# Kernel tuning notes

Hardware: AMD Instinct MI355X
Metric: run time of the kernel (lower is better)

## Reference

```python
import jax, jax.numpy as jnp
import numpy as np

NEG_BIG = -9.0e15  # mask value from original code (-9000000000000000.0)


def setup_inputs() -> dict:
    key = jax.random.key(0)
    k1, k2, k3, k4, k5 = jax.random.split(key, 5)
    B, N, M, D = 32, 1024, 1024, 128
    input1 = jax.random.normal(k1, (B, N, D), dtype=jnp.float32)
    input2 = jax.random.normal(k2, (B, M, D), dtype=jnp.float32)
    adj = jax.random.randint(k3, (B, N, M), 0, 2, dtype=jnp.int32)
    # xavier_normal on (D,1): std = gain*sqrt(2/(fan_in+fan_out)) = 1.414*sqrt(2/(D+1))
    std = 1.414 * np.sqrt(2.0 / (D + 1))
    a1 = jax.random.normal(k4, (D, 1), dtype=jnp.float32) * std
    a2 = jax.random.normal(k5, (D, 1), dtype=jnp.float32) * std
    return {"input1": input1, "input2": input2, "adj": adj, "a1": a1, "a2": a2}


def reference(input1, input2, adj, a1, a2):
    h, g = input1, input2
    # e1: (B,N,1), e2: (B,1,M); broadcast add replaces the repeat() calls
    e1 = jnp.matmul(h, a1)                      # (B,N,1)
    e2 = jnp.matmul(g, a2).transpose(0, 2, 1)   # (B,1,M)
    e = jax.nn.leaky_relu(e1 + e2, negative_slope=0.2)  # (B,N,M)
    attention = jnp.where(adj > 0, e, NEG_BIG)
    attention = jax.nn.softmax(attention, axis=2)
    attention = jnp.where(jnp.isnan(attention), 0.0, attention)
    # per-batch loop in original builds adj_[b,i,j] = adj[b,i,:].sum(); vectorized:
    deg = jnp.sum(adj, axis=2, keepdims=True).astype(attention.dtype)  # (B,N,1)
    attention = attention * deg
    h_prime = jnp.matmul(attention, g)          # (B,N,D)
    return h_prime
```

## Files before the change

### kernel.cpp

```cpp
#include <hip/hip_runtime.h>

#define BB 32
#define NN 1024
#define MM 1024
#define DD 128

typedef __attribute__((ext_vector_type(4))) float f32x4;
typedef __attribute__((ext_vector_type(8))) __bf16 bf16x8;
typedef unsigned short ushort_t;
typedef unsigned int uint_t;

#define L2E 1.44269504f

__device__ __forceinline__ unsigned f2bf(float x) {
    unsigned u = __builtin_bit_cast(unsigned, x);
    return (u + 0x7fffu + ((u >> 16) & 1u)) >> 16;
}

#define GLOAD16(gp, lp)                                                     \
    __builtin_amdgcn_global_load_lds(                                       \
        (const __attribute__((address_space(1))) unsigned int*)(gp),        \
        (__attribute__((address_space(3))) unsigned int*)(lp), 16, 0, 0)

__global__ __launch_bounds__(256) void prep(
    const float* __restrict__ g, const float* __restrict__ h,
    const float* __restrict__ a1, const float* __restrict__ a2,
    ushort_t* __restrict__ gq, float* __restrict__ e1,
    float* __restrict__ e2B, float* __restrict__ e2D)
{
    __shared__ ushort_t tl[DD][66];
    int b = blockIdx.y, m0 = blockIdx.x * 64, t = threadIdx.x;

    #pragma unroll
    for (int i = 0; i < 8; i++) {
        int idx = i * 256 + t;
        int m = idx >> 5;
        int c4 = (idx & 31) * 4;
        float4 v = *(const float4*)(h + ((size_t)(b * NN + m0 + m)) * DD + c4);
        float4 av = *(const float4*)(a1 + c4);
        float p = v.x * av.x + v.y * av.y + v.z * av.z + v.w * av.w;
        #pragma unroll
        for (int s = 16; s; s >>= 1) p += __shfl_xor(p, s);
        if ((t & 31) == 0) e1[b * NN + m0 + m] = p;
    }
    #pragma unroll
    for (int i = 0; i < 8; i++) {
        int idx = i * 256 + t;
        int m = idx >> 5;
        int c4 = (idx & 31) * 4;
        float4 v = *(const float4*)(g + ((size_t)(b * MM + m0 + m)) * DD + c4);
        tl[c4 + 0][m] = (ushort_t)f2bf(v.x);
        tl[c4 + 1][m] = (ushort_t)f2bf(v.y);
        tl[c4 + 2][m] = (ushort_t)f2bf(v.z);
        tl[c4 + 3][m] = (ushort_t)f2bf(v.w);
        float4 av = *(const float4*)(a2 + c4);
        float p = v.x * av.x + v.y * av.y + v.z * av.z + v.w * av.w;
        #pragma unroll
        for (int s = 16; s; s >>= 1) p += __shfl_xor(p, s);
        if ((t & 31) == 0) {
            e2B[b * MM + m0 + m] = __builtin_amdgcn_exp2f(L2E * p);
            e2D[b * MM + m0 + m] = __builtin_amdgcn_exp2f(0.2f * L2E * p);
        }
    }
    __syncthreads();
    #pragma unroll
    for (int i = 0; i < 4; i++) {
        int idx = i * 256 + t;
        int d = idx >> 3;
        int c = (idx & 7) * 8;
        int4 o;
        o.x = (int)((unsigned)tl[d][c + 0] | ((unsigned)tl[d][c + 1] << 16));
        o.y = (int)((unsigned)tl[d][c + 2] | ((unsigned)tl[d][c + 3] << 16));
        o.z = (int)((unsigned)tl[d][c + 4] | ((unsigned)tl[d][c + 5] << 16));
        o.w = (int)((unsigned)tl[d][c + 6] | ((unsigned)tl[d][c + 7] << 16));
        int mg = m0 + c;
        *(int4*)(gq + (((size_t)((b * 32 + (mg >> 5)) * DD + d)) << 5) + (mg & 31)) = o;
    }
}

__global__ __launch_bounds__(256, 2) void attn_tiled(
    const int* __restrict__ adj, const ushort_t* __restrict__ gq,
    const float* __restrict__ e1, const float* __restrict__ e2B,
    const float* __restrict__ e2D, float* __restrict__ out)
{
    __shared__ __align__(16) float BfS[MM];
    __shared__ __align__(16) float DfS[MM];
    __shared__ __align__(16) int adjS[4][64 * 32];
    __shared__ __align__(16) ushort_t gqS[4][128 * 32];

    int b = blockIdx.y, n0 = blockIdx.x * 64, t = threadIdx.x;
    int wid = t >> 6, lane = t & 63;
    int rlo = lane & 15, hh = lane >> 4;
    int r = wid * 16 + rlo;
    int r8 = r & 7;

    *(float4*)(&BfS[t * 4]) = *(const float4*)(e2B + b * MM + t * 4);
    *(float4*)(&DfS[t * 4]) = *(const float4*)(e2D + b * MM + t * 4);
    float e1r = e1[b * NN + n0 + r];
    float An   = __builtin_amdgcn_exp2f(L2E * e1r);
    float Cn   = __builtin_amdgcn_exp2f(0.2f * L2E * e1r);
    float invA = __builtin_amdgcn_exp2f(-L2E * e1r);
    __syncthreads();

    const int* adjb = adj + (size_t)(b * NN + n0) * MM;
    const ushort_t* gqb = gq + (size_t)b * (32 * DD * 32);

    int adi0 = t, adi1 = t + 256;
    int arow0 = adi0 >> 3, aseg0 = (adi0 & 7) ^ (arow0 & 7);
    int arow1 = adi1 >> 3, aseg1 = (adi1 & 7) ^ (arow1 & 7);
    int gd0 = adi0 >> 2, gseg0 = (adi0 & 3) ^ ((gd0 >> 1) & 3);
    int gd1 = adi1 >> 2, gseg1 = (adi1 & 3) ^ ((gd1 >> 1) & 3);

#define STAGE(P, K) do {                                                    \
        GLOAD16(adjb + (size_t)arow0 * MM + (K) * 32 + aseg0 * 4,           \
                &adjS[P][adi0 * 4]);                                        \
        GLOAD16(adjb + (size_t)arow1 * MM + (K) * 32 + aseg1 * 4,           \
                &adjS[P][adi1 * 4]);                                        \
        GLOAD16(gqb + (size_t)(K) * 4096 + gd0 * 32 + gseg0 * 8,            \
                &gqS[P][adi0 * 8]);                                         \
        GLOAD16(gqb + (size_t)(K) * 4096 + gd1 * 32 + gseg1 * 8,            \
                &gqS[P][adi1 * 8]);                                         \
    } while (0)

    f32x4 acc[8];
    #pragma unroll
    for (int j = 0; j < 8; j++) acc[j] = (f32x4){0.f, 0.f, 0.f, 0.f};
    float zl = 0.f;
    int dcnt = 0;

#define COMPUTE(P, K) do {                                                  \
        int4 a0 = *(const int4*)(&adjS[P][r * 32 + ((2 * hh) ^ r8) * 4]);   \
        int4 a1 = *(const int4*)(&adjS[P][r * 32 + ((2 * hh + 1) ^ r8) * 4]);\
        float4 b0 = *(const float4*)(&BfS[(K) * 32 + 8 * hh]);              \
        float4 b1 = *(const float4*)(&BfS[(K) * 32 + 8 * hh + 4]);          \
        float4 d0 = *(const float4*)(&DfS[(K) * 32 + 8 * hh]);              \
        float4 d1 = *(const float4*)(&DfS[(K) * 32 + 8 * hh + 4]);          \
        float Bv[8] = {b0.x, b0.y, b0.z, b0.w, b1.x, b1.y, b1.z, b1.w};     \
        float Dv[8] = {d0.x, d0.y, d0.z, d0.w, d1.x, d1.y, d1.z, d1.w};     \
        int   ax[8] = {a0.x, a0.y, a0.z, a0.w, a1.x, a1.y, a1.z, a1.w};     \
        bf16x8 af;                                                          \
        _Pragma("unroll")                                                   \
        for (int jj = 0; jj < 8; jj++) {                                    \
            float val = (Bv[jj] > invA) ? Bv[jj] * An : Dv[jj] * Cn;        \
            float wv = (ax[jj] > 0) ? val : 0.f;                            \
            zl += wv;                                                       \
            dcnt += ax[jj];                                                 \
            af[jj] = (__bf16)wv;                                            \
        }                                                                   \
        _Pragma("unroll")                                                   \
        for (int j = 0; j < 8; j++) {                                       \
            int d = j * 16 + rlo;                                           \
            int4 bv = *(const int4*)(                                       \
                &gqS[P][d * 32 + (hh ^ ((rlo >> 1) & 3)) * 8]);             \
            acc[j] = __builtin_amdgcn_mfma_f32_16x16x32_bf16(               \
                         af, __builtin_bit_cast(bf16x8, bv), acc[j], 0,0,0);\
        }                                                                   \
    } while (0)

    STAGE(0, 0); STAGE(1, 1); STAGE(2, 2);

    for (int k = 0; k < 30; ++k) {
        asm volatile("s_waitcnt vmcnt(8)" ::: "memory");
        __builtin_amdgcn_s_barrier();
        __builtin_amdgcn_sched_barrier(0);
        if (k < 29) STAGE((k + 3) & 3, k + 3);
        COMPUTE(k & 3, k);
    }
    asm volatile("s_waitcnt vmcnt(4)" ::: "memory");
    __builtin_amdgcn_s_barrier();
    __builtin_amdgcn_sched_barrier(0);
    COMPUTE(2, 30);
    asm volatile("s_waitcnt vmcnt(0)" ::: "memory");
    __builtin_amdgcn_s_barrier();
    __builtin_amdgcn_sched_barrier(0);
    COMPUTE(3, 31);

#undef COMPUTE
#undef STAGE

    zl += __shfl_xor(zl, 16); zl += __shfl_xor(zl, 32);
    dcnt += __shfl_xor(dcnt, 16); dcnt += __shfl_xor(dcnt, 32);
    float sc = (dcnt > 0) ? ((float)dcnt / zl) : 0.f;

    float scr[4];
    #pragma unroll
    for (int rg = 0; rg < 4; rg++) scr[rg] = __shfl(sc, 4 * hh + rg);

    float* ob = out + ((size_t)(b * NN + n0 + wid * 16)) * DD + rlo;
    #pragma unroll
    for (int j = 0; j < 8; j++)
        #pragma unroll
        for (int rg = 0; rg < 4; rg++)
            ob[(size_t)(4 * hh + rg) * DD + j * 16] = acc[j][rg] * scr[rg];
}

extern "C" void kernel_launch(void* const* d_in, const int* in_sizes, int n_in,
                              void* d_out, int out_size, void* d_ws, size_t ws_size,
                              hipStream_t stream) {
    const float* h   = (const float*)d_in[0];
    const float* g   = (const float*)d_in[1];
    const int*   adj = (const int*)d_in[2];
    const float* a1  = (const float*)d_in[3];
    const float* a2  = (const float*)d_in[4];
    float* out = (float*)d_out;

    char* ws = (char*)d_ws;
    float*    e1  = (float*)(ws);
    float*    e2B = (float*)(ws + (128u << 10));
    float*    e2D = (float*)(ws + (256u << 10));
    ushort_t* gq  = (ushort_t*)(ws + (512u << 10));

    prep<<<dim3(MM / 64, BB), 256, 0, stream>>>(g, h, a1, a2, gq, e1, e2B, e2D);
    attn_tiled<<<dim3(NN / 64, BB), 256, 0, stream>>>(adj, gq, e1, e2B, e2D, out);
}
```

Measured before the change: 48.15 us.

## Switch to double-buffered 64-wide K tiles with one barrier per two MFMA steps

```diff
diff --git a/kernel.cpp b/kernel.cpp
--- a/kernel.cpp
+++ b/kernel.cpp
@@ -85,14 +85,13 @@
 {
     __shared__ __align__(16) float BfS[MM];
     __shared__ __align__(16) float DfS[MM];
-    __shared__ __align__(16) int adjS[4][64 * 32];
-    __shared__ __align__(16) ushort_t gqS[4][128 * 32];
+    __shared__ __align__(16) int adjS[2][64 * 64];
+    __shared__ __align__(16) ushort_t gqS[2][2 * 128 * 32];
 
     int b = blockIdx.y, n0 = blockIdx.x * 64, t = threadIdx.x;
     int wid = t >> 6, lane = t & 63;
     int rlo = lane & 15, hh = lane >> 4;
     int r = wid * 16 + rlo;
-    int r8 = r & 7;
 
     *(float4*)(&BfS[t * 4]) = *(const float4*)(e2B + b * MM + t * 4);
     *(float4*)(&DfS[t * 4]) = *(const float4*)(e2D + b * MM + t * 4);
@@ -105,21 +104,32 @@
     const int* adjb = adj + (size_t)(b * NN + n0) * MM;
     const ushort_t* gqb = gq + (size_t)b * (32 * DD * 32);
 
-    int adi0 = t, adi1 = t + 256;
-    int arow0 = adi0 >> 3, aseg0 = (adi0 & 7) ^ (arow0 & 7);
-    int arow1 = adi1 >> 3, aseg1 = (adi1 & 7) ^ (arow1 & 7);
-    int gd0 = adi0 >> 2, gseg0 = (adi0 & 3) ^ ((gd0 >> 1) & 3);
-    int gd1 = adi1 >> 2, gseg1 = (adi1 & 3) ^ ((gd1 >> 1) & 3);
+    int adi[4], aoff[4];
+    #pragma unroll
+    for (int i = 0; i < 4; i++) {
+        adi[i] = t + i * 256;
+        int arow = adi[i] >> 4, aseg = (adi[i] & 15) ^ (arow & 15);
+        aoff[i] = arow * MM + aseg * 4;
+    }
+    int gtile[4], goff[4];
+    #pragma unroll
+    for (int i = 0; i < 4; i++) {
+        int di = t + i * 256;
+        gtile[i] = di >> 9;
+        int idx = di & 511;
+        int gd = idx >> 2, gseg = (idx & 3) ^ ((gd >> 1) & 3);
+        goff[i] = gd * 32 + gseg * 8;
+    }
 
 #define STAGE(P, K) do {                                                    \
-        GLOAD16(adjb + (size_t)arow0 * MM + (K) * 32 + aseg0 * 4,           \
-                &adjS[P][adi0 * 4]);                                        \
-        GLOAD16(adjb + (size_t)arow1 * MM + (K) * 32 + aseg1 * 4,           \
-                &adjS[P][adi1 * 4]);                                        \
-        GLOAD16(gqb + (size_t)(K) * 4096 + gd0 * 32 + gseg0 * 8,            \
-                &gqS[P][adi0 * 8]);                                         \
-        GLOAD16(gqb + (size_t)(K) * 4096 + gd1 * 32 + gseg1 * 8,            \
-                &gqS[P][adi1 * 8]);                                         \
+        _Pragma("unroll")                                                   \
+        for (int i = 0; i < 4; i++)                                         \
+            GLOAD16(adjb + (size_t)aoff[i] + (K) * 64,                      \
+                    &adjS[P][adi[i] * 4]);                                  \
+        _Pragma("unroll")                                                   \
+        for (int i = 0; i < 4; i++)                                         \
+            GLOAD16(gqb + (size_t)(2 * (K) + gtile[i]) * 4096 + goff[i],    \
+                    &gqS[P][(t + i * 256) * 8]);                            \
     } while (0)
 
     f32x4 acc[8];
@@ -128,13 +138,16 @@
     float zl = 0.f;
     int dcnt = 0;
 
-#define COMPUTE(P, K) do {                                                  \
-        int4 a0 = *(const int4*)(&adjS[P][r * 32 + ((2 * hh) ^ r8) * 4]);   \
-        int4 a1 = *(const int4*)(&adjS[P][r * 32 + ((2 * hh + 1) ^ r8) * 4]);\
-        float4 b0 = *(const float4*)(&BfS[(K) * 32 + 8 * hh]);              \
-        float4 b1 = *(const float4*)(&BfS[(K) * 32 + 8 * hh + 4]);          \
-        float4 d0 = *(const float4*)(&DfS[(K) * 32 + 8 * hh]);              \
-        float4 d1 = *(const float4*)(&DfS[(K) * 32 + 8 * hh + 4]);          \
+#define KSTEP(P, K, KS) do {                                                \
+        int4 a0 = *(const int4*)(                                           \
+            &adjS[P][r * 64 + (((KS) * 8 + 2 * hh) ^ rlo) * 4]);            \
+        int4 a1 = *(const int4*)(                                           \
+            &adjS[P][r * 64 + (((KS) * 8 + 2 * hh + 1) ^ rlo) * 4]);        \
+        int mo = (K) * 64 + (KS) * 32 + 8 * hh;                             \
+        float4 b0 = *(const float4*)(&BfS[mo]);                             \
+        float4 b1 = *(const float4*)(&BfS[mo + 4]);                         \
+        float4 d0 = *(const float4*)(&DfS[mo]);                             \
+        float4 d1 = *(const float4*)(&DfS[mo + 4]);                         \
         float Bv[8] = {b0.x, b0.y, b0.z, b0.w, b1.x, b1.y, b1.z, b1.w};     \
         float Dv[8] = {d0.x, d0.y, d0.z, d0.w, d1.x, d1.y, d1.z, d1.w};     \
         int   ax[8] = {a0.x, a0.y, a0.z, a0.w, a1.x, a1.y, a1.z, a1.w};     \
@@ -150,32 +163,25 @@
         _Pragma("unroll")                                                   \
         for (int j = 0; j < 8; j++) {                                       \
             int d = j * 16 + rlo;                                           \
-            int4 bv = *(const int4*)(                                       \
-                &gqS[P][d * 32 + (hh ^ ((rlo >> 1) & 3)) * 8]);             \
+            int4 bv = *(const int4*)(&gqS[P][(KS) * 4096 + d * 32 +         \
+                                             (hh ^ ((rlo >> 1) & 3)) * 8]); \
             acc[j] = __builtin_amdgcn_mfma_f32_16x16x32_bf16(               \
                          af, __builtin_bit_cast(bf16x8, bv), acc[j], 0,0,0);\
         }                                                                   \
     } while (0)
 
-    STAGE(0, 0); STAGE(1, 1); STAGE(2, 2);
-
-    for (int k = 0; k < 30; ++k) {
-        asm volatile("s_waitcnt vmcnt(8)" ::: "memory");
+    STAGE(0, 0);
+
+    for (int k = 0; k < 16; ++k) {
+        asm volatile("s_waitcnt vmcnt(0)" ::: "memory");
         __builtin_amdgcn_s_barrier();
         __builtin_amdgcn_sched_barrier(0);
-        if (k < 29) STAGE((k + 3) & 3, k + 3);
-        COMPUTE(k & 3, k);
-    }
-    asm volatile("s_waitcnt vmcnt(4)" ::: "memory");
-    __builtin_amdgcn_s_barrier();
-    __builtin_amdgcn_sched_barrier(0);
-    COMPUTE(2, 30);
-    asm volatile("s_waitcnt vmcnt(0)" ::: "memory");
-    __builtin_amdgcn_s_barrier();
-    __builtin_amdgcn_sched_barrier(0);
-    COMPUTE(3, 31);
-
-#undef COMPUTE
+        if (k < 15) STAGE((k + 1) & 1, k + 1);
+        KSTEP(k & 1, k, 0);
+        KSTEP(k & 1, k, 1);
+    }
+
+#undef KSTEP
 #undef STAGE
 
     zl += __shfl_xor(zl, 16); zl += __shfl_xor(zl, 32);
```

Measured after the change: 50.28 us. +4.4%, slower.

## Split M reduction across two thread halves with 512-thread blocks

Applied to the files above, without the earlier changes.

```diff
diff --git a/kernel.cpp b/kernel.cpp
--- a/kernel.cpp
+++ b/kernel.cpp
@@ -78,48 +78,51 @@
     }
 }
 
-__global__ __launch_bounds__(256, 2) void attn_tiled(
+__global__ __launch_bounds__(512, 4) void attn_tiled(
     const int* __restrict__ adj, const ushort_t* __restrict__ gq,
     const float* __restrict__ e1, const float* __restrict__ e2B,
     const float* __restrict__ e2D, float* __restrict__ out)
 {
     __shared__ __align__(16) float BfS[MM];
     __shared__ __align__(16) float DfS[MM];
-    __shared__ __align__(16) int adjS[4][64 * 32];
-    __shared__ __align__(16) ushort_t gqS[4][128 * 32];
+    __shared__ __align__(16) int adjS[2][2][64 * 32];
+    __shared__ __align__(16) ushort_t gqS[2][2][128 * 32];
 
     int b = blockIdx.y, n0 = blockIdx.x * 64, t = threadIdx.x;
-    int wid = t >> 6, lane = t & 63;
+    int half = t >> 8;
+    int tt = t & 255;
+    int wid4 = tt >> 6, lane = t & 63;
     int rlo = lane & 15, hh = lane >> 4;
-    int r = wid * 16 + rlo;
-    int r8 = r & 7;
-
-    *(float4*)(&BfS[t * 4]) = *(const float4*)(e2B + b * MM + t * 4);
-    *(float4*)(&DfS[t * 4]) = *(const float4*)(e2D + b * MM + t * 4);
+    int r = wid4 * 16 + rlo;
+    int c0 = half * 16;
+
+    if (half == 0)
+        *(float4*)(&BfS[tt * 4]) = *(const float4*)(e2B + b * MM + tt * 4);
+    else
+        *(float4*)(&DfS[tt * 4]) = *(const float4*)(e2D + b * MM + tt * 4);
     float e1r = e1[b * NN + n0 + r];
     float An   = __builtin_amdgcn_exp2f(L2E * e1r);
     float Cn   = __builtin_amdgcn_exp2f(0.2f * L2E * e1r);
     float invA = __builtin_amdgcn_exp2f(-L2E * e1r);
-    __syncthreads();
 
     const int* adjb = adj + (size_t)(b * NN + n0) * MM;
     const ushort_t* gqb = gq + (size_t)b * (32 * DD * 32);
 
-    int adi0 = t, adi1 = t + 256;
+    int adi0 = tt, adi1 = tt + 256;
     int arow0 = adi0 >> 3, aseg0 = (adi0 & 7) ^ (arow0 & 7);
     int arow1 = adi1 >> 3, aseg1 = (adi1 & 7) ^ (arow1 & 7);
     int gd0 = adi0 >> 2, gseg0 = (adi0 & 3) ^ ((gd0 >> 1) & 3);
     int gd1 = adi1 >> 2, gseg1 = (adi1 & 3) ^ ((gd1 >> 1) & 3);
 
-#define STAGE(P, K) do {                                                    \
-        GLOAD16(adjb + (size_t)arow0 * MM + (K) * 32 + aseg0 * 4,           \
-                &adjS[P][adi0 * 4]);                                        \
-        GLOAD16(adjb + (size_t)arow1 * MM + (K) * 32 + aseg1 * 4,           \
-                &adjS[P][adi1 * 4]);                                        \
-        GLOAD16(gqb + (size_t)(K) * 4096 + gd0 * 32 + gseg0 * 8,            \
-                &gqS[P][adi0 * 8]);                                         \
-        GLOAD16(gqb + (size_t)(K) * 4096 + gd1 * 32 + gseg1 * 8,            \
-                &gqS[P][adi1 * 8]);                                         \
+#define STAGE(P, C) do {                                                    \
+        GLOAD16(adjb + (size_t)arow0 * MM + (C) * 32 + aseg0 * 4,           \
+                &adjS[half][P][adi0 * 4]);                                  \
+        GLOAD16(adjb + (size_t)arow1 * MM + (C) * 32 + aseg1 * 4,           \
+                &adjS[half][P][adi1 * 4]);                                  \
+        GLOAD16(gqb + (size_t)(C) * 4096 + gd0 * 32 + gseg0 * 8,            \
+                &gqS[half][P][adi0 * 8]);                                   \
+        GLOAD16(gqb + (size_t)(C) * 4096 + gd1 * 32 + gseg1 * 8,            \
+                &gqS[half][P][adi1 * 8]);                                   \
     } while (0)
 
     f32x4 acc[8];
@@ -127,17 +130,21 @@
     for (int j = 0; j < 8; j++) acc[j] = (f32x4){0.f, 0.f, 0.f, 0.f};
     float zl = 0.f;
     int dcnt = 0;
-
-#define COMPUTE(P, K) do {                                                  \
-        int4 a0 = *(const int4*)(&adjS[P][r * 32 + ((2 * hh) ^ r8) * 4]);   \
-        int4 a1 = *(const int4*)(&adjS[P][r * 32 + ((2 * hh + 1) ^ r8) * 4]);\
-        float4 b0 = *(const float4*)(&BfS[(K) * 32 + 8 * hh]);              \
-        float4 b1 = *(const float4*)(&BfS[(K) * 32 + 8 * hh + 4]);          \
-        float4 d0 = *(const float4*)(&DfS[(K) * 32 + 8 * hh]);              \
-        float4 d1 = *(const float4*)(&DfS[(K) * 32 + 8 * hh + 4]);          \
+    int r8 = r & 7;
+
+#define COMPUTE(P, C) do {                                                  \
+        int4 a0 = *(const int4*)(&adjS[half][P][r * 32 + ((2*hh) ^ r8)*4]); \
+        int4 av1 = *(const int4*)(                                          \
+            &adjS[half][P][r * 32 + ((2*hh + 1) ^ r8) * 4]);                \
+        int mo = (C) * 32 + 8 * hh;                                         \
+        float4 b0 = *(const float4*)(&BfS[mo]);                             \
+        float4 b1 = *(const float4*)(&BfS[mo + 4]);                         \
+        float4 d0 = *(const float4*)(&DfS[mo]);                             \
+        float4 d1 = *(const float4*)(&DfS[mo + 4]);                         \
         float Bv[8] = {b0.x, b0.y, b0.z, b0.w, b1.x, b1.y, b1.z, b1.w};     \
         float Dv[8] = {d0.x, d0.y, d0.z, d0.w, d1.x, d1.y, d1.z, d1.w};     \
-        int   ax[8] = {a0.x, a0.y, a0.z, a0.w, a1.x, a1.y, a1.z, a1.w};     \
+        int   ax[8] = {a0.x, a0.y, a0.z, a0.w,                              \
+                       av1.x, av1.y, av1.z, av1.w};                         \
         bf16x8 af;                                                          \
         _Pragma("unroll")                                                   \
         for (int jj = 0; jj < 8; jj++) {                                    \
@@ -150,48 +157,56 @@
         _Pragma("unroll")                                                   \
         for (int j = 0; j < 8; j++) {                                       \
             int d = j * 16 + rlo;                                           \
-            int4 bv = *(const int4*)(                                       \
-                &gqS[P][d * 32 + (hh ^ ((rlo >> 1) & 3)) * 8]);             \
+            int4 bv = *(const int4*)(&gqS[half][P][d * 32 +                 \
+                                     (hh ^ ((rlo >> 1) & 3)) * 8]);         \
             acc[j] = __builtin_amdgcn_mfma_f32_16x16x32_bf16(               \
                          af, __builtin_bit_cast(bf16x8, bv), acc[j], 0,0,0);\
         }                                                                   \
     } while (0)
 
-    STAGE(0, 0); STAGE(1, 1); STAGE(2, 2);
-
-    for (int k = 0; k < 30; ++k) {
-        asm volatile("s_waitcnt vmcnt(8)" ::: "memory");
+    STAGE(0, c0);
+    asm volatile("s_waitcnt vmcnt(0) lgkmcnt(0)" ::: "memory");
+    __builtin_amdgcn_s_barrier();
+
+    for (int k = 0; k < 16; ++k) {
+        if (k < 15) STAGE((k + 1) & 1, c0 + k + 1);
+        COMPUTE(k & 1, c0 + k);
+        asm volatile("s_waitcnt vmcnt(0)" ::: "memory");
         __builtin_amdgcn_s_barrier();
-        __builtin_amdgcn_sched_barrier(0);
-        if (k < 29) STAGE((k + 3) & 3, k + 3);
-        COMPUTE(k & 3, k);
-    }
-    asm volatile("s_waitcnt vmcnt(4)" ::: "memory");
-    __builtin_amdgcn_s_barrier();
-    __builtin_amdgcn_sched_barrier(0);
-    COMPUTE(2, 30);
-    asm volatile("s_waitcnt vmcnt(0)" ::: "memory");
-    __builtin_amdgcn_s_barrier();
-    __builtin_amdgcn_sched_barrier(0);
-    COMPUTE(3, 31);
+    }
 
 #undef COMPUTE
 #undef STAGE
 
-    zl += __shfl_xor(zl, 16); zl += __shfl_xor(zl, 32);
-    dcnt += __shfl_xor(dcnt, 16); dcnt += __shfl_xor(dcnt, 32);
-    float sc = (dcnt > 0) ? ((float)dcnt / zl) : 0.f;
-
-    float scr[4];
-    #pragma unroll
-    for (int rg = 0; rg < 4; rg++) scr[rg] = __shfl(sc, 4 * hh + rg);
-
-    float* ob = out + ((size_t)(b * NN + n0 + wid * 16)) * DD + rlo;
-    #pragma unroll
-    for (int j = 0; j < 8; j++)
-        #pragma unroll
-        for (int rg = 0; rg < 4; rg++)
-            ob[(size_t)(4 * hh + rg) * DD + j * 16] = acc[j][rg] * scr[rg];
+    f32x4* accS = (f32x4*)&adjS[0][0][0];
+    if (half == 1) {
+        #pragma unroll
+        for (int j = 0; j < 8; j++) accS[j * 256 + tt] = acc[j];
+        BfS[tt] = zl;
+        DfS[tt] = (float)dcnt;
+    }
+    __syncthreads();
+    if (half == 0) {
+        #pragma unroll
+        for (int j = 0; j < 8; j++) acc[j] += accS[j * 256 + tt];
+        zl += BfS[tt];
+        dcnt += (int)DfS[tt];
+
+        zl += __shfl_xor(zl, 16); zl += __shfl_xor(zl, 32);
+        dcnt += __shfl_xor(dcnt, 16); dcnt += __shfl_xor(dcnt, 32);
+        float sc = (dcnt > 0) ? ((float)dcnt / zl) : 0.f;
+
+        float scr[4];
+        #pragma unroll
+        for (int rg = 0; rg < 4; rg++) scr[rg] = __shfl(sc, 4 * hh + rg);
+
+        float* ob = out + ((size_t)(b * NN + n0 + wid4 * 16)) * DD + rlo;
+        #pragma unroll
+        for (int j = 0; j < 8; j++)
+            #pragma unroll
+            for (int rg = 0; rg < 4; rg++)
+                ob[(size_t)(4 * hh + rg) * DD + j * 16] = acc[j][rg] * scr[rg];
+    }
 }
 
 extern "C" void kernel_launch(void* const* d_in, const int* in_sizes, int n_in,
@@ -211,5 +226,5 @@
     ushort_t* gq  = (ushort_t*)(ws + (512u << 10));
 
     prep<<<dim3(MM / 64, BB), 256, 0, stream>>>(g, h, a1, a2, gq, e1, e2B, e2D);
-    attn_tiled<<<dim3(NN / 64, BB), 256, 0, stream>>>(adj, gq, e1, e2B, e2D, out);
-}
+    attn_tiled<<<dim3(NN / 64, BB), 512, 0, stream>>>(adj, gq, e1, e2B, e2D, out);
+}
```

Result: no change. 48.00 us, median of 2 (-0.3%).
